# Kernel tuning notes

Measured on AMD Instinct MI355X. Metric: run time of the kernel, lower is better.

Reference implementation:

```python
import jax, jax.numpy as jnp
import numpy as np

N_NODES = 100000
N_EDGES = 1600000
IN_CH = 64
OUT_CH = 64
N_CLASSES = 10


def setup_inputs() -> dict:
    key = jax.random.key(0)
    k1, k2, k3, k4 = jax.random.split(key, 4)
    x = jax.random.normal(k1, (N_NODES, IN_CH), dtype=jnp.float32)
    edge_index = jax.random.randint(k2, (2, N_EDGES), 0, N_NODES, dtype=jnp.int64)
    # Glorot-scaled weights like PyG GCNConv init
    W1 = jax.random.normal(k3, (IN_CH, OUT_CH), dtype=jnp.float32) * (1.0 / np.sqrt(IN_CH))
    b1 = jnp.zeros((OUT_CH,), dtype=jnp.float32)
    W2 = jax.random.normal(k4, (OUT_CH, N_CLASSES), dtype=jnp.float32) * (1.0 / np.sqrt(OUT_CH))
    b2 = jnp.zeros((N_CLASSES,), dtype=jnp.float32)
    return {"x": x, "W1": W1, "b1": b1, "W2": W2, "b2": b2, "edge_index": edge_index}


def _gcn_conv(x, W, b, src, dst, num_nodes):
    """PyG GCNConv: out = D^{-1/2} (A + I) D^{-1/2} (x W) + b."""
    h = x @ W  # [N, F_out] -- project first (PyG order)
    loops = jnp.arange(num_nodes, dtype=src.dtype)
    s = jnp.concatenate([src, loops])  # message sources j
    d = jnp.concatenate([dst, loops])  # message targets i
    deg = jax.ops.segment_sum(jnp.ones(s.shape, h.dtype), d, num_segments=num_nodes)
    deg_inv_sqrt = jnp.where(deg > 0, jax.lax.rsqrt(jnp.maximum(deg, 1.0)), 0.0)
    norm = deg_inv_sqrt[s] * deg_inv_sqrt[d]  # [E+N]
    msg = h[s] * norm[:, None]  # gather + normalize
    out = jax.ops.segment_sum(msg, d, num_segments=num_nodes)  # scatter-add
    return out + b


def reference(x, W1, b1, W2, b2, edge_index):
    src, dst = edge_index[0], edge_index[1]
    n = x.shape[0]
    h = _gcn_conv(x, W1, b1, src, dst, n)
    out = _gcn_conv(h, W2, b2, src, dst, n)
    return out
```

## Files before the change

### kernel.cpp

```cpp
#include <hip/hip_runtime.h>
#include <hip/hip_fp16.h>


#define NN 100000
#define NE 1600000
#define NPB 256
#define NB 391
#define CHUNK 4096
#define NCB 391
#define MAXB 5120

__global__ __launch_bounds__(256) void k_part(const int* __restrict__ src,
                                              const int* __restrict__ dst,
                                              const float* __restrict__ W1,
                                              const float* __restrict__ W2,
                                              const float* __restrict__ b1,
                                              int* __restrict__ packed,
                                              int* __restrict__ scanT,
                                              float* __restrict__ W12,
                                              float* __restrict__ c1) {
    __shared__ int hist[NB];
    __shared__ int sc[256];
    __shared__ int cur[NB];
    __shared__ int buf[CHUNK];
    int c = blockIdx.x, t = threadIdx.x;
    if (c == NCB) {
        for (int o = t; o < 640; o += 256) {
            int k = o / 10, ch = o - k * 10;
            float acc = 0.f;
            #pragma unroll
            for (int m = 0; m < 64; ++m) acc = fmaf(W1[k * 64 + m], W2[m * 10 + ch], acc);
            W12[o] = acc;
        }
        if (t < 10) {
            float acc = 0.f;
            #pragma unroll
            for (int m = 0; m < 64; ++m) acc = fmaf(b1[m], W2[m * 10 + t], acc);
            c1[t] = acc;
        }
        return;
    }
    int e0 = c * CHUNK, e1 = min(e0 + CHUNK, NE);
    int n = e1 - e0;
    for (int i = t; i < NB; i += 256) hist[i] = 0;
    __syncthreads();
    int pk[16], bk[16];
    #pragma unroll
    for (int k = 0; k < 16; ++k) {
        int e = e0 + t + k * 256;
        if (e < e1) {
            int s = src[e], d = dst[e];
            pk[k] = (s << 8) | (d & 255);
            bk[k] = d >> 8;
            atomicAdd(&hist[bk[k]], 1);
        } else bk[k] = -1;
    }
    __syncthreads();
    int i0 = 2 * t, i1 = 2 * t + 1;
    int h0 = (i0 < NB) ? hist[i0] : 0;
    int h1 = (i1 < NB) ? hist[i1] : 0;
    int ps = h0 + h1;
    sc[t] = ps; __syncthreads();
    for (int off = 1; off < 256; off <<= 1) {
        int a = (t >= off) ? sc[t - off] : 0;
        __syncthreads(); sc[t] += a; __syncthreads();
    }
    int exc = sc[t] - ps;
    if (i0 < NB) cur[i0] = exc;
    if (i1 < NB) cur[i1] = exc + h0;
    __syncthreads();
    for (int b = t; b < NB; b += 256) scanT[c * (NB + 1) + b] = e0 + cur[b];
    if (t == 0) scanT[c * (NB + 1) + NB] = e0 + n;
    __syncthreads();
    #pragma unroll
    for (int k = 0; k < 16; ++k) {
        if (bk[k] >= 0) {
            int pos = atomicAdd(&cur[bk[k]], 1);
            buf[pos] = pk[k];
        }
    }
    __syncthreads();
    for (int i = t; i < n; i += 256) packed[e0 + i] = buf[i];
}

__global__ __launch_bounds__(512) void k_sortproj(const int* __restrict__ packed,
                                                  const int* __restrict__ scanT,
                                                  const float* __restrict__ x,
                                                  const float* __restrict__ W12g,
                                                  int* __restrict__ ssrc,
                                                  int2* __restrict__ rowbe,
                                                  float* __restrict__ dis,
                                                  uint2* __restrict__ ydu) {
    __shared__ int stage[MAXB];
    __shared__ int sorted[MAXB];
    __shared__ int sstart[NCB];
    __shared__ int segoff[NCB + 1];
    __shared__ int sc512[512];
    __shared__ int cnt[NPB];
    __shared__ int sc[NPB];
    __shared__ int cur[NPB];
    __shared__ float disl[NPB];
    __shared__ float Wl[640];
    int b = blockIdx.x, t = threadIdx.x;
    int wbase = b * MAXB;

    if (t < NPB) cnt[t] = 0;
    int myl = 0;
    if (t < NCB) {
        int s0 = scanT[t * (NB + 1) + b];
        int s1 = scanT[t * (NB + 1) + b + 1];
        sstart[t] = s0;
        myl = s1 - s0;
    }
    sc512[t] = myl;
    __syncthreads();
    for (int off = 1; off < 512; off <<= 1) {
        int a = (t >= off) ? sc512[t - off] : 0;
        __syncthreads(); sc512[t] += a; __syncthreads();
    }
    if (t < NCB) segoff[t] = sc512[t] - myl;
    if (t == 0) segoff[NCB] = sc512[511];
    __syncthreads();
    int Tfull = sc512[511];
    int T = min(Tfull, MAXB);

    for (int i = t; i < Tfull; i += 512) {
        int lo = 0, hi = NCB;
        while (hi - lo > 1) {
            int mid = (lo + hi) >> 1;
            if (segoff[mid] <= i) lo = mid; else hi = mid;
        }
        int p = packed[sstart[lo] + (i - segoff[lo])];
        if (i < MAXB) stage[i] = p;
        atomicAdd(&cnt[p & 255], 1);
    }
    __syncthreads();
    if (t < NPB) sc[t] = cnt[t];
    __syncthreads();
    for (int off = 1; off < NPB; off <<= 1) {
        int a = 0;
        if (t < NPB && t >= off) a = sc[t - off];
        __syncthreads();
        if (t < NPB) sc[t] += a;
        __syncthreads();
    }
    if (t < NPB) {
        int h = cnt[t];
        int exc = sc[t] - h;
        int nidx = b * NPB + t;
        float dh = rsqrtf((float)h + 1.0f);
        disl[t] = dh;
        if (nidx < NN) {
            rowbe[nidx] = make_int2(wbase + min(exc, MAXB), wbase + min(exc + h, MAXB));
            dis[nidx] = dh;
        }
        cur[t] = exc;
    }
    for (int i = t; i < 640; i += 512) Wl[i] = W12g[i];
    __syncthreads();
    for (int i = t; i < T; i += 512) {
        int p = stage[i];
        int pos = atomicAdd(&cur[p & 255], 1);
        if (pos < MAXB) sorted[pos] = p;
    }
    __syncthreads();
    for (int i = t; i < T; i += 512) ssrc[wbase + i] = sorted[i] >> 8;
    __syncthreads();

    int r = t >> 1, h = t & 1;
    int n = b * NPB + r;
    if (n < NN) {
        const float* xr = &x[n * 64 + h * 32];
        float4 xa[8];
        #pragma unroll
        for (int i = 0; i < 8; ++i) xa[i] = *(const float4*)&xr[i * 4];
        float acc[10];
        #pragma unroll
        for (int ch = 0; ch < 10; ++ch) acc[ch] = 0.f;
        #pragma unroll
        for (int i = 0; i < 8; ++i) {
            int k0 = h * 32 + i * 4;
            #pragma unroll
            for (int ch = 0; ch < 10; ++ch) {
                acc[ch] = fmaf(xa[i].x, Wl[(k0 + 0) * 10 + ch], acc[ch]);
                acc[ch] = fmaf(xa[i].y, Wl[(k0 + 1) * 10 + ch], acc[ch]);
                acc[ch] = fmaf(xa[i].z, Wl[(k0 + 2) * 10 + ch], acc[ch]);
                acc[ch] = fmaf(xa[i].w, Wl[(k0 + 3) * 10 + ch], acc[ch]);
            }
        }
        #pragma unroll
        for (int ch = 0; ch < 10; ++ch) acc[ch] += __shfl_xor(acc[ch], 1);
        float dh = disl[r];
        if (h == 0) {
            __half2 p0 = __floats2half2_rn(dh * acc[0], dh * acc[1]);
            __half2 p1 = __floats2half2_rn(dh * acc[2], dh * acc[3]);
            uint2 w; w.x = *(unsigned*)&p0; w.y = *(unsigned*)&p1;
            ydu[n * 4 + 0] = w;
        } else {
            __half2 p0 = __floats2half2_rn(dh * acc[4], dh * acc[5]);
            __half2 p1 = __floats2half2_rn(dh * acc[6], dh * acc[7]);
            uint2 w; w.x = *(unsigned*)&p0; w.y = *(unsigned*)&p1;
            ydu[n * 4 + 1] = w;
            __half2 p2 = __floats2half2_rn(dh * acc[8], dh * acc[9]);
            __half2 p3 = __floats2half2_rn(dh, 0.f);
            uint2 w2; w2.x = *(unsigned*)&p2; w2.y = *(unsigned*)&p3;
            ydu[n * 4 + 2] = w2;
        }
    }
}

__device__ __forceinline__ float4 cvt4(uint2 v) {
    __half2 h0 = *(__half2*)&v.x, h1 = *(__half2*)&v.y;
    float2 f0 = __half22float2(h0), f1 = __half22float2(h1);
    return make_float4(f0.x, f0.y, f1.x, f1.y);
}

__global__ __launch_bounds__(256) void k_aggA(const uint2* __restrict__ ydu,
                                              const float* __restrict__ dis,
                                              const int2* __restrict__ rowbe,
                                              const int* __restrict__ ssrc,
                                              uint2* __restrict__ zdu) {
    int t = blockIdx.x * blockDim.x + threadIdx.x;
    int n = t >> 2, q = t & 3;
    if (n >= NN) return;
    int2 be = rowbe[n];
    const bool act = (q < 3);
    float4 a0 = make_float4(0.f, 0.f, 0.f, 0.f), a1 = a0, a2 = a0, a3 = a0;
    if (act) a0 = cvt4(ydu[n * 4 + q]);
    int j = be.x;
    for (; j + 3 < be.y; j += 4) {
        int s0 = ssrc[j], s1 = ssrc[j + 1], s2 = ssrc[j + 2], s3 = ssrc[j + 3];
        if (act) {
            float4 v0 = cvt4(ydu[s0 * 4 + q]);
            float4 v1 = cvt4(ydu[s1 * 4 + q]);
            float4 v2 = cvt4(ydu[s2 * 4 + q]);
            float4 v3 = cvt4(ydu[s3 * 4 + q]);
            a0.x += v0.x; a0.y += v0.y; a0.z += v0.z; a0.w += v0.w;
            a1.x += v1.x; a1.y += v1.y; a1.z += v1.z; a1.w += v1.w;
            a2.x += v2.x; a2.y += v2.y; a2.z += v2.z; a2.w += v2.w;
            a3.x += v3.x; a3.y += v3.y; a3.z += v3.z; a3.w += v3.w;
        }
    }
    for (; j < be.y; ++j) {
        int s = ssrc[j];
        if (act) {
            float4 v = cvt4(ydu[s * 4 + q]);
            a0.x += v.x; a0.y += v.y; a0.z += v.z; a0.w += v.w;
        }
    }
    if (act) {
        float4 s;
        s.x = (a0.x + a1.x) + (a2.x + a3.x);
        s.y = (a0.y + a1.y) + (a2.y + a3.y);
        s.z = (a0.z + a1.z) + (a2.z + a3.z);
        s.w = (a0.w + a1.w) + (a2.w + a3.w);
        float d = dis[n], d2 = d * d;
        __half2 lo, hi;
        if (q < 2) {
            lo = __floats2half2_rn(d2 * s.x, d2 * s.y);
            hi = __floats2half2_rn(d2 * s.z, d2 * s.w);
        } else {
            lo = __floats2half2_rn(d2 * s.x, d2 * s.y);
            hi = __floats2half2_rn(d * s.z, 0.f);
        }
        uint2 w; w.x = *(unsigned*)&lo; w.y = *(unsigned*)&hi;
        zdu[n * 4 + q] = w;
    }
}

__global__ __launch_bounds__(256) void k_aggB(const uint2* __restrict__ zdu,
                                              const float* __restrict__ dis,
                                              const int2* __restrict__ rowbe,
                                              const int* __restrict__ ssrc,
                                              const float* __restrict__ c1,
                                              const float* __restrict__ b2,
                                              float* __restrict__ out) {
    int t = blockIdx.x * blockDim.x + threadIdx.x;
    int n = t >> 2, q = t & 3;
    if (n >= NN) return;
    int2 be = rowbe[n];
    const bool act = (q < 3);
    float4 self = make_float4(0.f, 0.f, 0.f, 0.f);
    if (act) self = cvt4(zdu[n * 4 + q]);
    float4 a0 = self, a1 = make_float4(0.f, 0.f, 0.f, 0.f), a2 = a1, a3 = a1;
    int j = be.x;
    for (; j + 3 < be.y; j += 4) {
        int s0 = ssrc[j], s1 = ssrc[j + 1], s2 = ssrc[j + 2], s3 = ssrc[j + 3];
        if (act) {
            float4 v0 = cvt4(zdu[s0 * 4 + q]);
            float4 v1 = cvt4(zdu[s1 * 4 + q]);
            float4 v2 = cvt4(zdu[s2 * 4 + q]);
            float4 v3 = cvt4(zdu[s3 * 4 + q]);
            a0.x += v0.x; a0.y += v0.y; a0.z += v0.z; a0.w += v0.w;
            a1.x += v1.x; a1.y += v1.y; a1.z += v1.z; a1.w += v1.w;
            a2.x += v2.x; a2.y += v2.y; a2.z += v2.z; a2.w += v2.w;
            a3.x += v3.x; a3.y += v3.y; a3.z += v3.z; a3.w += v3.w;
        }
    }
    for (; j < be.y; ++j) {
        int s = ssrc[j];
        if (act) {
            float4 v = cvt4(zdu[s * 4 + q]);
            a0.x += v.x; a0.y += v.y; a0.z += v.z; a0.w += v.w;
        }
    }
    float4 s;
    s.x = (a0.x + a1.x) + (a2.x + a3.x);
    s.y = (a0.y + a1.y) + (a2.y + a3.y);
    s.z = (a0.z + a1.z) + (a2.z + a3.z);
    s.w = (a0.w + a1.w) + (a2.w + a3.w);
    float n1 = __shfl(self.z, 2, 4);
    float d = dis[n];
    if (q == 0) {
        out[n * 10 + 0] = fmaf(d, s.x, fmaf(n1, c1[0], b2[0]));
        out[n * 10 + 1] = fmaf(d, s.y, fmaf(n1, c1[1], b2[1]));
        out[n * 10 + 2] = fmaf(d, s.z, fmaf(n1, c1[2], b2[2]));
        out[n * 10 + 3] = fmaf(d, s.w, fmaf(n1, c1[3], b2[3]));
    } else if (q == 1) {
        out[n * 10 + 4] = fmaf(d, s.x, fmaf(n1, c1[4], b2[4]));
        out[n * 10 + 5] = fmaf(d, s.y, fmaf(n1, c1[5], b2[5]));
        out[n * 10 + 6] = fmaf(d, s.z, fmaf(n1, c1[6], b2[6]));
        out[n * 10 + 7] = fmaf(d, s.w, fmaf(n1, c1[7], b2[7]));
    } else if (q == 2) {
        out[n * 10 + 8] = fmaf(d, s.x, fmaf(n1, c1[8], b2[8]));
        out[n * 10 + 9] = fmaf(d, s.y, fmaf(n1, c1[9], b2[9]));
    }
}

extern "C" void kernel_launch(void* const* d_in, const int* in_sizes, int n_in,
                              void* d_out, int out_size, void* d_ws, size_t ws_size,
                              hipStream_t stream) {
    const float* x  = (const float*)d_in[0];
    const float* W1 = (const float*)d_in[1];
    const float* b1 = (const float*)d_in[2];
    const float* W2 = (const float*)d_in[3];
    const float* b2 = (const float*)d_in[4];
    const int* edge = (const int*)d_in[5];
    const int* src = edge;
    const int* dst = edge + NE;
    float* out = (float*)d_out;

    char* W = (char*)d_ws;
    uint2* ydu    = (uint2*)(W);
    uint2* zdu    = (uint2*)(W + 3200000);
    float* dis    = (float*)(W + 6400000);
    int*   packed = (int*)  (W + 6800000);
    int*   scanT  = (int*)  (W + 13200000);
    int*   ssrc   = (int*)  (W + 13813120);
    int2*  rowbe  = (int2*) (W + 21820800);
    float* W12    = (float*)(W + 22620800);
    float* c1     = (float*)(W + 22623360);

    k_part    <<<NCB + 1, 256, 0, stream>>>(src, dst, W1, W2, b1, packed, scanT, W12, c1);
    k_sortproj<<<NB, 512, 0, stream>>>(packed, scanT, x, W12, ssrc, rowbe, dis, ydu);
    k_aggA    <<<(NN * 4 + 255) / 256, 256, 0, stream>>>(ydu, dis, rowbe, ssrc, zdu);
    k_aggB    <<<(NN * 4 + 255) / 256, 256, 0, stream>>>(zdu, dis, rowbe, ssrc, c1, b2, out);
}
```

Before: 72.50 us.

## Use two 16-byte lanes per node in aggregation and wave-level scans in sort

The aggregation kernels switch from four threads per node, each gathering 8 bytes with one thread idle, to two threads per node, each gathering 16 bytes. This halves thread count and removes the idle lane. In k_sortproj the block-wide Hillis-Steele scans become wave shuffle scans, and the histogram is split into per-wave counters to cut atomic contention. The shared-memory sorted buffer is dropped and sorted sources are scattered directly to global memory. The cost is more registers per thread and uncoalesced global scatter writes.

```diff
diff --git a/kernel.cpp b/kernel.cpp
--- a/kernel.cpp
+++ b/kernel.cpp
@@ -90,21 +90,22 @@
                                                   int* __restrict__ ssrc,
                                                   int2* __restrict__ rowbe,
                                                   float* __restrict__ dis,
-                                                  uint2* __restrict__ ydu) {
+                                                  uint4* __restrict__ ydu) {
     __shared__ int stage[MAXB];
-    __shared__ int sorted[MAXB];
     __shared__ int sstart[NCB];
     __shared__ int segoff[NCB + 1];
-    __shared__ int sc512[512];
-    __shared__ int cnt[NPB];
-    __shared__ int sc[NPB];
+    __shared__ int wtot[8];
+    __shared__ int cnt8[8][NPB];
     __shared__ int cur[NPB];
     __shared__ float disl[NPB];
     __shared__ float Wl[640];
+    __shared__ int totsh;
     int b = blockIdx.x, t = threadIdx.x;
+    int lane = t & 63, w = t >> 6;
     int wbase = b * MAXB;
 
-    if (t < NPB) cnt[t] = 0;
+    for (int i = t; i < 8 * NPB; i += 512) ((int*)cnt8)[i] = 0;
+
     int myl = 0;
     if (t < NCB) {
         int s0 = scanT[t * (NB + 1) + b];
@@ -112,16 +113,25 @@
         sstart[t] = s0;
         myl = s1 - s0;
     }
-    sc512[t] = myl;
-    __syncthreads();
-    for (int off = 1; off < 512; off <<= 1) {
-        int a = (t >= off) ? sc512[t - off] : 0;
-        __syncthreads(); sc512[t] += a; __syncthreads();
-    }
-    if (t < NCB) segoff[t] = sc512[t] - myl;
-    if (t == 0) segoff[NCB] = sc512[511];
-    __syncthreads();
-    int Tfull = sc512[511];
+    int v = myl;
+    #pragma unroll
+    for (int off = 1; off < 64; off <<= 1) {
+        int u = __shfl_up(v, off);
+        if (lane >= off) v += u;
+    }
+    if (lane == 63) wtot[w] = v;
+    __syncthreads();
+    if (t == 0) {
+        int s = 0;
+        #pragma unroll
+        for (int i = 0; i < 8; ++i) { int xx = wtot[i]; wtot[i] = s; s += xx; }
+        totsh = s;
+    }
+    __syncthreads();
+    if (t < NCB) segoff[t] = v + wtot[w] - myl;
+    if (t == 0) segoff[NCB] = totsh;
+    __syncthreads();
+    int Tfull = totsh;
     int T = min(Tfull, MAXB);
 
     for (int i = t; i < Tfull; i += 512) {
@@ -132,39 +142,50 @@
         }
         int p = packed[sstart[lo] + (i - segoff[lo])];
         if (i < MAXB) stage[i] = p;
-        atomicAdd(&cnt[p & 255], 1);
-    }
-    __syncthreads();
-    if (t < NPB) sc[t] = cnt[t];
-    __syncthreads();
-    for (int off = 1; off < NPB; off <<= 1) {
-        int a = 0;
-        if (t < NPB && t >= off) a = sc[t - off];
-        __syncthreads();
-        if (t < NPB) sc[t] += a;
-        __syncthreads();
-    }
+        atomicAdd(&cnt8[w][p & 255], 1);
+    }
+    __syncthreads();
+    int hsum = 0, incl = 0;
     if (t < NPB) {
-        int h = cnt[t];
-        int exc = sc[t] - h;
+        #pragma unroll
+        for (int i = 0; i < 8; ++i) hsum += cnt8[i][t];
+        int vv = hsum;
+        #pragma unroll
+        for (int off = 1; off < 64; off <<= 1) {
+            int u = __shfl_up(vv, off);
+            if (lane >= off) vv += u;
+        }
+        if (lane == 63) wtot[w] = vv;
+        incl = vv;
+    }
+    __syncthreads();
+    if (t == 0) {
+        int s = 0;
+        #pragma unroll
+        for (int i = 0; i < 4; ++i) { int xx = wtot[i]; wtot[i] = s; s += xx; }
+    }
+    __syncthreads();
+    if (t < NPB) {
+        int exc = incl + wtot[w] - hsum;
         int nidx = b * NPB + t;
-        float dh = rsqrtf((float)h + 1.0f);
+        float dh = rsqrtf((float)hsum + 1.0f);
         disl[t] = dh;
         if (nidx < NN) {
-            rowbe[nidx] = make_int2(wbase + min(exc, MAXB), wbase + min(exc + h, MAXB));
+            rowbe[nidx] = make_int2(wbase + min(exc, MAXB), wbase + min(exc + hsum, MAXB));
             dis[nidx] = dh;
         }
-        cur[t] = exc;
+        cur[t] = wbase + exc;
     }
     for (int i = t; i < 640; i += 512) Wl[i] = W12g[i];
     __syncthreads();
-    for (int i = t; i < T; i += 512) {
-        int p = stage[i];
-        int pos = atomicAdd(&cur[p & 255], 1);
-        if (pos < MAXB) sorted[pos] = p;
-    }
-    __syncthreads();
-    for (int i = t; i < T; i += 512) ssrc[wbase + i] = sorted[i] >> 8;
+    {
+        int wlim = wbase + MAXB;
+        for (int i = t; i < T; i += 512) {
+            int p = stage[i];
+            int pos = atomicAdd(&cur[p & 255], 1);
+            if (pos < wlim) ssrc[pos] = p >> 8;
+        }
+    }
     __syncthreads();
 
     int r = t >> 1, h = t & 1;
@@ -191,84 +212,90 @@
         #pragma unroll
         for (int ch = 0; ch < 10; ++ch) acc[ch] += __shfl_xor(acc[ch], 1);
         float dh = disl[r];
+        uint4 wv;
         if (h == 0) {
             __half2 p0 = __floats2half2_rn(dh * acc[0], dh * acc[1]);
             __half2 p1 = __floats2half2_rn(dh * acc[2], dh * acc[3]);
-            uint2 w; w.x = *(unsigned*)&p0; w.y = *(unsigned*)&p1;
-            ydu[n * 4 + 0] = w;
+            __half2 p2 = __floats2half2_rn(dh * acc[4], dh * acc[5]);
+            __half2 p3 = __floats2half2_rn(dh * acc[6], dh * acc[7]);
+            wv.x = *(unsigned*)&p0; wv.y = *(unsigned*)&p1;
+            wv.z = *(unsigned*)&p2; wv.w = *(unsigned*)&p3;
+            ydu[n * 2 + 0] = wv;
         } else {
-            __half2 p0 = __floats2half2_rn(dh * acc[4], dh * acc[5]);
-            __half2 p1 = __floats2half2_rn(dh * acc[6], dh * acc[7]);
-            uint2 w; w.x = *(unsigned*)&p0; w.y = *(unsigned*)&p1;
-            ydu[n * 4 + 1] = w;
-            __half2 p2 = __floats2half2_rn(dh * acc[8], dh * acc[9]);
-            __half2 p3 = __floats2half2_rn(dh, 0.f);
-            uint2 w2; w2.x = *(unsigned*)&p2; w2.y = *(unsigned*)&p3;
-            ydu[n * 4 + 2] = w2;
-        }
-    }
-}
-
-__device__ __forceinline__ float4 cvt4(uint2 v) {
+            __half2 p0 = __floats2half2_rn(dh * acc[8], dh * acc[9]);
+            __half2 p1 = __floats2half2_rn(dh, 0.f);
+            __half2 pz = __floats2half2_rn(0.f, 0.f);
+            wv.x = *(unsigned*)&p0; wv.y = *(unsigned*)&p1;
+            wv.z = *(unsigned*)&pz; wv.w = *(unsigned*)&pz;
+            ydu[n * 2 + 1] = wv;
+        }
+    }
+}
+
+__device__ __forceinline__ void cvt8(uint4 v, float* f) {
     __half2 h0 = *(__half2*)&v.x, h1 = *(__half2*)&v.y;
-    float2 f0 = __half22float2(h0), f1 = __half22float2(h1);
-    return make_float4(f0.x, f0.y, f1.x, f1.y);
-}
-
-__global__ __launch_bounds__(256) void k_aggA(const uint2* __restrict__ ydu,
+    __half2 h2 = *(__half2*)&v.z, h3 = *(__half2*)&v.w;
+    float2 a = __half22float2(h0), b = __half22float2(h1);
+    float2 c = __half22float2(h2), d = __half22float2(h3);
+    f[0] = a.x; f[1] = a.y; f[2] = b.x; f[3] = b.y;
+    f[4] = c.x; f[5] = c.y; f[6] = d.x; f[7] = d.y;
+}
+
+__global__ __launch_bounds__(256) void k_aggA(const uint4* __restrict__ ydu,
                                               const float* __restrict__ dis,
                                               const int2* __restrict__ rowbe,
                                               const int* __restrict__ ssrc,
-                                              uint2* __restrict__ zdu) {
+                                              uint4* __restrict__ zdu) {
     int t = blockIdx.x * blockDim.x + threadIdx.x;
-    int n = t >> 2, q = t & 3;
+    int n = t >> 1, h = t & 1;
     if (n >= NN) return;
     int2 be = rowbe[n];
-    const bool act = (q < 3);
-    float4 a0 = make_float4(0.f, 0.f, 0.f, 0.f), a1 = a0, a2 = a0, a3 = a0;
-    if (act) a0 = cvt4(ydu[n * 4 + q]);
+    float a0[8], a1[8], a2[8], a3[8];
+    cvt8(ydu[n * 2 + h], a0);
+    #pragma unroll
+    for (int i = 0; i < 8; ++i) { a1[i] = 0.f; a2[i] = 0.f; a3[i] = 0.f; }
     int j = be.x;
     for (; j + 3 < be.y; j += 4) {
         int s0 = ssrc[j], s1 = ssrc[j + 1], s2 = ssrc[j + 2], s3 = ssrc[j + 3];
-        if (act) {
-            float4 v0 = cvt4(ydu[s0 * 4 + q]);
-            float4 v1 = cvt4(ydu[s1 * 4 + q]);
-            float4 v2 = cvt4(ydu[s2 * 4 + q]);
-            float4 v3 = cvt4(ydu[s3 * 4 + q]);
-            a0.x += v0.x; a0.y += v0.y; a0.z += v0.z; a0.w += v0.w;
-            a1.x += v1.x; a1.y += v1.y; a1.z += v1.z; a1.w += v1.w;
-            a2.x += v2.x; a2.y += v2.y; a2.z += v2.z; a2.w += v2.w;
-            a3.x += v3.x; a3.y += v3.y; a3.z += v3.z; a3.w += v3.w;
+        float v0[8], v1[8], v2[8], v3[8];
+        cvt8(ydu[s0 * 2 + h], v0);
+        cvt8(ydu[s1 * 2 + h], v1);
+        cvt8(ydu[s2 * 2 + h], v2);
+        cvt8(ydu[s3 * 2 + h], v3);
+        #pragma unroll
+        for (int i = 0; i < 8; ++i) {
+            a0[i] += v0[i]; a1[i] += v1[i]; a2[i] += v2[i]; a3[i] += v3[i];
         }
     }
     for (; j < be.y; ++j) {
-        int s = ssrc[j];
-        if (act) {
-            float4 v = cvt4(ydu[s * 4 + q]);
-            a0.x += v.x; a0.y += v.y; a0.z += v.z; a0.w += v.w;
-        }
-    }
-    if (act) {
-        float4 s;
-        s.x = (a0.x + a1.x) + (a2.x + a3.x);
-        s.y = (a0.y + a1.y) + (a2.y + a3.y);
-        s.z = (a0.z + a1.z) + (a2.z + a3.z);
-        s.w = (a0.w + a1.w) + (a2.w + a3.w);
-        float d = dis[n], d2 = d * d;
-        __half2 lo, hi;
-        if (q < 2) {
-            lo = __floats2half2_rn(d2 * s.x, d2 * s.y);
-            hi = __floats2half2_rn(d2 * s.z, d2 * s.w);
-        } else {
-            lo = __floats2half2_rn(d2 * s.x, d2 * s.y);
-            hi = __floats2half2_rn(d * s.z, 0.f);
-        }
-        uint2 w; w.x = *(unsigned*)&lo; w.y = *(unsigned*)&hi;
-        zdu[n * 4 + q] = w;
-    }
-}
-
-__global__ __launch_bounds__(256) void k_aggB(const uint2* __restrict__ zdu,
+        float v[8];
+        cvt8(ydu[ssrc[j] * 2 + h], v);
+        #pragma unroll
+        for (int i = 0; i < 8; ++i) a0[i] += v[i];
+    }
+    float s[8];
+    #pragma unroll
+    for (int i = 0; i < 8; ++i) s[i] = (a0[i] + a1[i]) + (a2[i] + a3[i]);
+    float d = dis[n], d2 = d * d;
+    uint4 wv;
+    if (h == 0) {
+        __half2 p0 = __floats2half2_rn(d2 * s[0], d2 * s[1]);
+        __half2 p1 = __floats2half2_rn(d2 * s[2], d2 * s[3]);
+        __half2 p2 = __floats2half2_rn(d2 * s[4], d2 * s[5]);
+        __half2 p3 = __floats2half2_rn(d2 * s[6], d2 * s[7]);
+        wv.x = *(unsigned*)&p0; wv.y = *(unsigned*)&p1;
+        wv.z = *(unsigned*)&p2; wv.w = *(unsigned*)&p3;
+    } else {
+        __half2 p0 = __floats2half2_rn(d2 * s[0], d2 * s[1]);
+        __half2 p1 = __floats2half2_rn(d * s[2], 0.f);
+        __half2 pz = __floats2half2_rn(0.f, 0.f);
+        wv.x = *(unsigned*)&p0; wv.y = *(unsigned*)&p1;
+        wv.z = *(unsigned*)&pz; wv.w = *(unsigned*)&pz;
+    }
+    zdu[n * 2 + h] = wv;
+}
+
+__global__ __launch_bounds__(256) void k_aggB(const uint4* __restrict__ zdu,
                                               const float* __restrict__ dis,
                                               const int2* __restrict__ rowbe,
                                               const int* __restrict__ ssrc,
@@ -276,54 +303,52 @@
                                               const float* __restrict__ b2,
                                               float* __restrict__ out) {
     int t = blockIdx.x * blockDim.x + threadIdx.x;
-    int n = t >> 2, q = t & 3;
+    int n = t >> 1, h = t & 1;
     if (n >= NN) return;
     int2 be = rowbe[n];
-    const bool act = (q < 3);
-    float4 self = make_float4(0.f, 0.f, 0.f, 0.f);
-    if (act) self = cvt4(zdu[n * 4 + q]);
-    float4 a0 = self, a1 = make_float4(0.f, 0.f, 0.f, 0.f), a2 = a1, a3 = a1;
+    float a0[8], a1[8], a2[8], a3[8];
+    cvt8(zdu[n * 2 + h], a0);
+    float selfn1 = a0[2];
+    #pragma unroll
+    for (int i = 0; i < 8; ++i) { a1[i] = 0.f; a2[i] = 0.f; a3[i] = 0.f; }
     int j = be.x;
     for (; j + 3 < be.y; j += 4) {
         int s0 = ssrc[j], s1 = ssrc[j + 1], s2 = ssrc[j + 2], s3 = ssrc[j + 3];
-        if (act) {
-            float4 v0 = cvt4(zdu[s0 * 4 + q]);
-            float4 v1 = cvt4(zdu[s1 * 4 + q]);
-            float4 v2 = cvt4(zdu[s2 * 4 + q]);
-            float4 v3 = cvt4(zdu[s3 * 4 + q]);
-            a0.x += v0.x; a0.y += v0.y; a0.z += v0.z; a0.w += v0.w;
-            a1.x += v1.x; a1.y += v1.y; a1.z += v1.z; a1.w += v1.w;
-            a2.x += v2.x; a2.y += v2.y; a2.z += v2.z; a2.w += v2.w;
-            a3.x += v3.x; a3.y += v3.y; a3.z += v3.z; a3.w += v3.w;
+        float v0[8], v1[8], v2[8], v3[8];
+        cvt8(zdu[s0 * 2 + h], v0);
+        cvt8(zdu[s1 * 2 + h], v1);
+        cvt8(zdu[s2 * 2 + h], v2);
+        cvt8(zdu[s3 * 2 + h], v3);
+        #pragma unroll
+        for (int i = 0; i < 8; ++i) {
+            a0[i] += v0[i]; a1[i] += v1[i]; a2[i] += v2[i]; a3[i] += v3[i];
         }
     }
     for (; j < be.y; ++j) {
-        int s = ssrc[j];
-        if (act) {
-            float4 v = cvt4(zdu[s * 4 + q]);
-            a0.x += v.x; a0.y += v.y; a0.z += v.z; a0.w += v.w;
-        }
-    }
-    float4 s;
-    s.x = (a0.x + a1.x) + (a2.x + a3.x);
-    s.y = (a0.y + a1.y) + (a2.y + a3.y);
-    s.z = (a0.z + a1.z) + (a2.z + a3.z);
-    s.w = (a0.w + a1.w) + (a2.w + a3.w);
-    float n1 = __shfl(self.z, 2, 4);
+        float v[8];
+        cvt8(zdu[ssrc[j] * 2 + h], v);
+        #pragma unroll
+        for (int i = 0; i < 8; ++i) a0[i] += v[i];
+    }
+    float s[8];
+    #pragma unroll
+    for (int i = 0; i < 8; ++i) s[i] = (a0[i] + a1[i]) + (a2[i] + a3[i]);
+    float n1 = __shfl(selfn1, 1, 2);
     float d = dis[n];
-    if (q == 0) {
-        out[n * 10 + 0] = fmaf(d, s.x, fmaf(n1, c1[0], b2[0]));
-        out[n * 10 + 1] = fmaf(d, s.y, fmaf(n1, c1[1], b2[1]));
-        out[n * 10 + 2] = fmaf(d, s.z, fmaf(n1, c1[2], b2[2]));
-        out[n * 10 + 3] = fmaf(d, s.w, fmaf(n1, c1[3], b2[3]));
-    } else if (q == 1) {
-        out[n * 10 + 4] = fmaf(d, s.x, fmaf(n1, c1[4], b2[4]));
-        out[n * 10 + 5] = fmaf(d, s.y, fmaf(n1, c1[5], b2[5]));
-        out[n * 10 + 6] = fmaf(d, s.z, fmaf(n1, c1[6], b2[6]));
-        out[n * 10 + 7] = fmaf(d, s.w, fmaf(n1, c1[7], b2[7]));
-    } else if (q == 2) {
-        out[n * 10 + 8] = fmaf(d, s.x, fmaf(n1, c1[8], b2[8]));
-        out[n * 10 + 9] = fmaf(d, s.y, fmaf(n1, c1[9], b2[9]));
+    if (h == 0) {
+        float2* o = (float2*)&out[n * 10];
+        o[0] = make_float2(fmaf(d, s[0], fmaf(n1, c1[0], b2[0])),
+                           fmaf(d, s[1], fmaf(n1, c1[1], b2[1])));
+        o[1] = make_float2(fmaf(d, s[2], fmaf(n1, c1[2], b2[2])),
+                           fmaf(d, s[3], fmaf(n1, c1[3], b2[3])));
+        o[2] = make_float2(fmaf(d, s[4], fmaf(n1, c1[4], b2[4])),
+                           fmaf(d, s[5], fmaf(n1, c1[5], b2[5])));
+        o[3] = make_float2(fmaf(d, s[6], fmaf(n1, c1[6], b2[6])),
+                           fmaf(d, s[7], fmaf(n1, c1[7], b2[7])));
+    } else {
+        *(float2*)&out[n * 10 + 8] =
+            make_float2(fmaf(d, s[0], fmaf(n1, c1[8], b2[8])),
+                        fmaf(d, s[1], fmaf(n1, c1[9], b2[9])));
     }
 }
 
@@ -341,8 +366,8 @@
     float* out = (float*)d_out;
 
     char* W = (char*)d_ws;
-    uint2* ydu    = (uint2*)(W);
-    uint2* zdu    = (uint2*)(W + 3200000);
+    uint4* ydu    = (uint4*)(W);
+    uint4* zdu    = (uint4*)(W + 3200000);
     float* dis    = (float*)(W + 6400000);
     int*   packed = (int*)  (W + 6800000);
     int*   scanT  = (int*)  (W + 13200000);
@@ -353,6 +378,6 @@
 
     k_part    <<<NCB + 1, 256, 0, stream>>>(src, dst, W1, W2, b1, packed, scanT, W12, c1);
     k_sortproj<<<NB, 512, 0, stream>>>(packed, scanT, x, W12, ssrc, rowbe, dis, ydu);
-    k_aggA    <<<(NN * 4 + 255) / 256, 256, 0, stream>>>(ydu, dis, rowbe, ssrc, zdu);
-    k_aggB    <<<(NN * 4 + 255) / 256, 256, 0, stream>>>(zdu, dis, rowbe, ssrc, c1, b2, out);
-}
+    k_aggA    <<<(NN * 2 + 255) / 256, 256, 0, stream>>>(ydu, dis, rowbe, ssrc, zdu);
+    k_aggB    <<<(NN * 2 + 255) / 256, 256, 0, stream>>>(zdu, dis, rowbe, ssrc, c1, b2, out);
+}
```

After: 76.78 us, median of 2. 1.06x slower.

## Use wave-shuffle scans and per-wave histograms in sort kernel; scatter directly to global

Applied to the files above, without the earlier changes.

Replaces the barrier-heavy shared-memory prefix scans in k_sortproj with wave-level __shfl_up scans plus a small cross-wave combine. The destination-node histogram is split into eight per-wave copies to reduce LDS atomic contention. The LDS 'sorted' staging buffer is dropped in favour of scattering source indices straight into global ssrc. The projected-feature stores become two 16-byte writes per node in place of three 8-byte writes, keeping the same byte layout and zero-filling the padding. The scatter now issues uncoalesced global writes, and the histogram reduction adds extra LDS reads.

```diff
diff --git a/kernel.cpp b/kernel.cpp
--- a/kernel.cpp
+++ b/kernel.cpp
@@ -90,21 +90,22 @@
                                                   int* __restrict__ ssrc,
                                                   int2* __restrict__ rowbe,
                                                   float* __restrict__ dis,
-                                                  uint2* __restrict__ ydu) {
+                                                  uint4* __restrict__ ydu) {
     __shared__ int stage[MAXB];
-    __shared__ int sorted[MAXB];
     __shared__ int sstart[NCB];
     __shared__ int segoff[NCB + 1];
-    __shared__ int sc512[512];
-    __shared__ int cnt[NPB];
-    __shared__ int sc[NPB];
+    __shared__ int wtot[8];
+    __shared__ int cnt8[8][NPB];
     __shared__ int cur[NPB];
     __shared__ float disl[NPB];
     __shared__ float Wl[640];
+    __shared__ int totsh;
     int b = blockIdx.x, t = threadIdx.x;
+    int lane = t & 63, w = t >> 6;
     int wbase = b * MAXB;
 
-    if (t < NPB) cnt[t] = 0;
+    for (int i = t; i < 8 * NPB; i += 512) ((int*)cnt8)[i] = 0;
+
     int myl = 0;
     if (t < NCB) {
         int s0 = scanT[t * (NB + 1) + b];
@@ -112,16 +113,25 @@
         sstart[t] = s0;
         myl = s1 - s0;
     }
-    sc512[t] = myl;
-    __syncthreads();
-    for (int off = 1; off < 512; off <<= 1) {
-        int a = (t >= off) ? sc512[t - off] : 0;
-        __syncthreads(); sc512[t] += a; __syncthreads();
-    }
-    if (t < NCB) segoff[t] = sc512[t] - myl;
-    if (t == 0) segoff[NCB] = sc512[511];
-    __syncthreads();
-    int Tfull = sc512[511];
+    int v = myl;
+    #pragma unroll
+    for (int off = 1; off < 64; off <<= 1) {
+        int u = __shfl_up(v, off);
+        if (lane >= off) v += u;
+    }
+    if (lane == 63) wtot[w] = v;
+    __syncthreads();
+    if (t == 0) {
+        int s = 0;
+        #pragma unroll
+        for (int i = 0; i < 8; ++i) { int xx = wtot[i]; wtot[i] = s; s += xx; }
+        totsh = s;
+    }
+    __syncthreads();
+    if (t < NCB) segoff[t] = v + wtot[w] - myl;
+    if (t == 0) segoff[NCB] = totsh;
+    __syncthreads();
+    int Tfull = totsh;
     int T = min(Tfull, MAXB);
 
     for (int i = t; i < Tfull; i += 512) {
@@ -132,39 +142,50 @@
         }
         int p = packed[sstart[lo] + (i - segoff[lo])];
         if (i < MAXB) stage[i] = p;
-        atomicAdd(&cnt[p & 255], 1);
-    }
-    __syncthreads();
-    if (t < NPB) sc[t] = cnt[t];
-    __syncthreads();
-    for (int off = 1; off < NPB; off <<= 1) {
-        int a = 0;
-        if (t < NPB && t >= off) a = sc[t - off];
-        __syncthreads();
-        if (t < NPB) sc[t] += a;
-        __syncthreads();
-    }
+        atomicAdd(&cnt8[w][p & 255], 1);
+    }
+    __syncthreads();
+    int hsum = 0, incl = 0;
     if (t < NPB) {
-        int h = cnt[t];
-        int exc = sc[t] - h;
+        #pragma unroll
+        for (int i = 0; i < 8; ++i) hsum += cnt8[i][t];
+        int vv = hsum;
+        #pragma unroll
+        for (int off = 1; off < 64; off <<= 1) {
+            int u = __shfl_up(vv, off);
+            if (lane >= off) vv += u;
+        }
+        if (lane == 63) wtot[w] = vv;
+        incl = vv;
+    }
+    __syncthreads();
+    if (t == 0) {
+        int s = 0;
+        #pragma unroll
+        for (int i = 0; i < 4; ++i) { int xx = wtot[i]; wtot[i] = s; s += xx; }
+    }
+    __syncthreads();
+    if (t < NPB) {
+        int exc = incl + wtot[w] - hsum;
         int nidx = b * NPB + t;
-        float dh = rsqrtf((float)h + 1.0f);
+        float dh = rsqrtf((float)hsum + 1.0f);
         disl[t] = dh;
         if (nidx < NN) {
-            rowbe[nidx] = make_int2(wbase + min(exc, MAXB), wbase + min(exc + h, MAXB));
+            rowbe[nidx] = make_int2(wbase + min(exc, MAXB), wbase + min(exc + hsum, MAXB));
             dis[nidx] = dh;
         }
-        cur[t] = exc;
+        cur[t] = wbase + exc;
     }
     for (int i = t; i < 640; i += 512) Wl[i] = W12g[i];
     __syncthreads();
-    for (int i = t; i < T; i += 512) {
-        int p = stage[i];
-        int pos = atomicAdd(&cur[p & 255], 1);
-        if (pos < MAXB) sorted[pos] = p;
-    }
-    __syncthreads();
-    for (int i = t; i < T; i += 512) ssrc[wbase + i] = sorted[i] >> 8;
+    {
+        int wlim = wbase + MAXB;
+        for (int i = t; i < T; i += 512) {
+            int p = stage[i];
+            int pos = atomicAdd(&cur[p & 255], 1);
+            if (pos < wlim) ssrc[pos] = p >> 8;
+        }
+    }
     __syncthreads();
 
     int r = t >> 1, h = t & 1;
@@ -191,20 +212,22 @@
         #pragma unroll
         for (int ch = 0; ch < 10; ++ch) acc[ch] += __shfl_xor(acc[ch], 1);
         float dh = disl[r];
+        uint4 wv;
         if (h == 0) {
             __half2 p0 = __floats2half2_rn(dh * acc[0], dh * acc[1]);
             __half2 p1 = __floats2half2_rn(dh * acc[2], dh * acc[3]);
-            uint2 w; w.x = *(unsigned*)&p0; w.y = *(unsigned*)&p1;
-            ydu[n * 4 + 0] = w;
+            __half2 p2 = __floats2half2_rn(dh * acc[4], dh * acc[5]);
+            __half2 p3 = __floats2half2_rn(dh * acc[6], dh * acc[7]);
+            wv.x = *(unsigned*)&p0; wv.y = *(unsigned*)&p1;
+            wv.z = *(unsigned*)&p2; wv.w = *(unsigned*)&p3;
+            ydu[n * 2 + 0] = wv;
         } else {
-            __half2 p0 = __floats2half2_rn(dh * acc[4], dh * acc[5]);
-            __half2 p1 = __floats2half2_rn(dh * acc[6], dh * acc[7]);
-            uint2 w; w.x = *(unsigned*)&p0; w.y = *(unsigned*)&p1;
-            ydu[n * 4 + 1] = w;
-            __half2 p2 = __floats2half2_rn(dh * acc[8], dh * acc[9]);
-            __half2 p3 = __floats2half2_rn(dh, 0.f);
-            uint2 w2; w2.x = *(unsigned*)&p2; w2.y = *(unsigned*)&p3;
-            ydu[n * 4 + 2] = w2;
+            __half2 p0 = __floats2half2_rn(dh * acc[8], dh * acc[9]);
+            __half2 p1 = __floats2half2_rn(dh, 0.f);
+            __half2 pz = __floats2half2_rn(0.f, 0.f);
+            wv.x = *(unsigned*)&p0; wv.y = *(unsigned*)&p1;
+            wv.z = *(unsigned*)&pz; wv.w = *(unsigned*)&pz;
+            ydu[n * 2 + 1] = wv;
         }
     }
 }
@@ -341,8 +364,8 @@
     float* out = (float*)d_out;
 
     char* W = (char*)d_ws;
-    uint2* ydu    = (uint2*)(W);
-    uint2* zdu    = (uint2*)(W + 3200000);
+    uint4* ydu    = (uint4*)(W);
+    uint4* zdu    = (uint4*)(W + 3200000);
     float* dis    = (float*)(W + 6400000);
     int*   packed = (int*)  (W + 6800000);
     int*   scanT  = (int*)  (W + 13200000);
@@ -353,6 +376,6 @@
 
     k_part    <<<NCB + 1, 256, 0, stream>>>(src, dst, W1, W2, b1, packed, scanT, W12, c1);
     k_sortproj<<<NB, 512, 0, stream>>>(packed, scanT, x, W12, ssrc, rowbe, dis, ydu);
-    k_aggA    <<<(NN * 4 + 255) / 256, 256, 0, stream>>>(ydu, dis, rowbe, ssrc, zdu);
-    k_aggB    <<<(NN * 4 + 255) / 256, 256, 0, stream>>>(zdu, dis, rowbe, ssrc, c1, b2, out);
-}
+    k_aggA    <<<(NN * 4 + 255) / 256, 256, 0, stream>>>((const uint2*)ydu, dis, rowbe, ssrc, (uint2*)zdu);
+    k_aggB    <<<(NN * 4 + 255) / 256, 256, 0, stream>>>((const uint2*)zdu, dis, rowbe, ssrc, c1, b2, out);
+}
```

Result: slower. 75.22 us (+3.8%).
